# Kernel optimization log

Measured on AMD Instinct MI355X. Metric: run time of the kernel, lower is better.

Reference implementation:

```python
import jax, jax.numpy as jnp
import numpy as np
import math

HIDDEN = 256
INPUT_SIZE = 32

def setup_inputs() -> dict:
    key = jax.random.key(0)
    k1, k2, k3 = jax.random.split(key, 3)
    stdv = 1.0 / math.sqrt(HIDDEN)
    inp = jax.random.normal(k1, (32, 48, 24, INPUT_SIZE), dtype=jnp.float32)
    W = jax.random.uniform(k2, (6 * HIDDEN, INPUT_SIZE + 2 * HIDDEN), minval=-stdv, maxval=stdv, dtype=jnp.float32)
    Bp = jax.random.uniform(k3, (6 * HIDDEN,), minval=-stdv, maxval=stdv, dtype=jnp.float32)
    return {"input": inp, "W": W, "Bp": Bp}

def _witran_forward(input, W, Bp):
    B, rows, cols, C = input.shape
    H = W.shape[0] // 6
    # flag == 1: permute to (cols, batch, rows, C)
    x = jnp.transpose(input, (2, 0, 1, 3))
    R = cols            # Water2sea_slice_num
    Lorig = rows        # Original_slice_len
    L = R + Lorig - 1   # Water2sea_slice_len
    # input_transfer: row r occupies slice positions r : r+Lorig (pad then roll)
    padded = jnp.pad(x, ((0, 0), (0, 0), (0, R - 1), (0, 0)))        # (R, B, L, C)
    shifted = jax.vmap(lambda xr, r: jnp.roll(xr, r, axis=1))(padded, jnp.arange(R))
    a = shifted.reshape(R * B, L, C)
    a_slices = jnp.transpose(a, (1, 0, 2))                            # (L, R*B, C)
    r_idx = jnp.repeat(jnp.arange(R), B)                              # (R*B,)

    def step(carry, inp):
        h_row, h_col = carry
        s, xs = inp
        # bias applied only to first (s+1)*B rows and only while s < R (faithful to torch)
        mask = ((r_idx <= s) & (s < R)).astype(xs.dtype)[:, None]
        gate = jnp.concatenate([h_row, h_col, xs], axis=-1) @ W.T + mask * Bp
        sig = jax.nn.sigmoid(gate[:, : 4 * H])
        tg = jnp.tanh(gate[:, 4 * H:])
        u_row, o_row, u_col, o_col = jnp.split(sig, 4, axis=-1)
        i_row, i_col = jnp.split(tg, 2, axis=-1)
        h_row = jnp.tanh((1.0 - u_row) * h_row + u_row * i_row) * o_row
        h_col_new = jnp.tanh((1.0 - u_col) * h_col + u_col * i_col) * o_col
        # roll col hidden down by one batch block for next diagonal
        h_col_rolled = jnp.roll(h_col_new, B, axis=0)
        return (h_row, h_col_rolled), (h_row, h_col_new)

    init = (jnp.zeros((R * B, H), input.dtype), jnp.zeros((R * B, H), input.dtype))
    _, (rows_all, cols_all) = jax.lax.scan(step, init, (jnp.arange(L), a_slices))
    # output_all_slice: stack along slice dim -> (R*B, L, 2H)
    output_all = jnp.transpose(jnp.concatenate([rows_all, cols_all], axis=-1), (1, 0, 2))
    rows_r = rows_all.reshape(L, R, B, H)
    cols_r = cols_all.reshape(L, R, B, H)
    # row hidden saved at slice s = Lorig-1+k from block k (diagonal)
    hidden_row = rows_r[jnp.arange(Lorig - 1, L), jnp.arange(R)]      # (R, B, H)
    # col hidden saved at slices s >= R-1 from the last block (pre-roll)
    hidden_col = cols_r[R - 1:, R - 1]                                # (Lorig, B, H)
    hidden_row_all = jnp.transpose(hidden_row, (1, 0, 2)).reshape(B, 1, R, H)
    hidden_col_all = jnp.transpose(hidden_col, (1, 0, 2)).reshape(B, 1, Lorig, H)
    # flag == 1 return order: (output, hidden_col_all, hidden_row_all)
    return output_all, hidden_col_all, hidden_row_all

def reference(input, W, Bp):
    return _witran_forward(input, W, Bp)
```

## Files before the change

kernel.cpp:

```cpp
#include <hip/hip_runtime.h>
#include <cstddef>


namespace {
constexpr int H_   = 256;
constexpr int C_   = 32;
constexpr int B_   = 32;
constexpr int R_   = 24;
constexpr int LOR_ = 48;
constexpr int L_   = 71;
constexpr int N_   = 768;
constexpr int KH_  = 512;
constexpr int KT_  = 544;
constexpr int AST_ = 552;
}

typedef __attribute__((ext_vector_type(8))) _Float16       f16x8;
typedef __attribute__((ext_vector_type(8))) unsigned short u16x8;
typedef __attribute__((ext_vector_type(4))) float          f32x4;
typedef __attribute__((ext_vector_type(2))) float          f32x2;

__device__ __forceinline__ float fsig(float x)  { return 1.f / (1.f + __expf(-x)); }
__device__ __forceinline__ float ftanhf(float x){ float e = __expf(2.f * x); return 1.f - 2.f / (e + 1.f); }

__global__ __launch_bounds__(256) void prep_w(const float* __restrict__ W,
                                              _Float16* __restrict__ Wfrag) {
    int o = blockIdx.x * 256 + threadIdx.x;
    int j8   = o & 7;
    int lane = (o >> 3) & 63;
    int rest = o >> 9;
    int lt   = rest % 96;
    int kc   = rest / 96;
    int n0 = lane & 15, quad = lane >> 4;
    int lg  = lt * 16 + n0;
    int kt  = lg / 96;
    int rem = lg % 96;
    int g  = rem >> 4, kl = rem & 15;
    int j  = g * 256 + kt * 16 + kl;
    int kg = kc * 32 + quad * 8 + j8;
    Wfrag[o] = (_Float16)W[j * KT_ + kg];
}

__global__ __launch_bounds__(256) void prep_x(const float* __restrict__ inp,
                                              _Float16* __restrict__ xall) {
    int o = blockIdx.x * 256 + threadIdx.x;
    int c = o & 31;
    int n = (o >> 5) % N_;
    int s = (o >> 5) / N_;
    int r = n >> 5, b = n & 31;
    int l = s - r;
    float v = 0.f;
    if (l >= 0 && l < LOR_) v = inp[((b * LOR_ + l) * R_ + r) * C_ + c];
    xall[o] = (_Float16)v;
}

__global__ __launch_bounds__(384, 2) void step_k(
    const _Float16* __restrict__ Wfrag,
    const _Float16* __restrict__ xall,
    const _Float16* __restrict__ hbc,
    const float*    __restrict__ hfc,
    _Float16*       __restrict__ hbn,
    float*          __restrict__ hfn,
    const float* __restrict__ Bp,
    float* __restrict__ out0, float* __restrict__ out1, float* __restrict__ out2,
    int s)
{
    __shared__ unsigned short As[48 * AST_];
    __shared__ float Gt[48][104];

    const int t    = threadIdx.x;
    const int wv   = t >> 6;
    const int lane = t & 63;
    const int n0   = lane & 15;
    const int quad = lane >> 4;
    const int kt   = blockIdx.x & 15;
    const int mc   = blockIdx.x >> 4;

#pragma unroll
    for (int it = 0; it < 8; ++it) {
        int q   = it * 384 + t;
        int row = q >> 6;
        int col = (q & 63) * 8;
        *(u16x8*)(void*)(&As[row * AST_ + col]) =
            *(const u16x8*)(const void*)((const unsigned short*)hbc +
                                         (size_t)(mc * 48 + row) * KH_ + col);
    }
    if (t < 192) {
        int row = t >> 2;
        int col = (t & 3) * 8;
        *(u16x8*)(void*)(&As[row * AST_ + 512 + col]) =
            *(const u16x8*)(const void*)((const unsigned short*)xall +
                                         (size_t)(s * N_ + mc * 48 + row) * C_ + col);
    }
    __syncthreads();

    f32x4 acc[3];
#pragma unroll
    for (int mt = 0; mt < 3; ++mt) acc[mt] = (f32x4){0.f, 0.f, 0.f, 0.f};

#pragma unroll
    for (int kc = 0; kc < 17; ++kc) {
        f16x8 b = *(const f16x8*)(const void*)(
            Wfrag + ((size_t)(kc * 96 + kt * 6 + wv) * 64 + lane) * 8);
        f16x8 a[3];
#pragma unroll
        for (int mt = 0; mt < 3; ++mt)
            a[mt] = *(const f16x8*)(const void*)(
                &As[(mt * 16 + n0) * AST_ + kc * 32 + quad * 8]);
#pragma unroll
        for (int mt = 0; mt < 3; ++mt)
            acc[mt] = __builtin_amdgcn_mfma_f32_16x16x32_f16(a[mt], b, acc[mt], 0, 0, 0);
    }

#pragma unroll
    for (int mt = 0; mt < 3; ++mt)
#pragma unroll
        for (int reg = 0; reg < 4; ++reg)
            Gt[mt * 16 + quad * 4 + reg][wv * 16 + n0] = acc[mt][reg];

    __syncthreads();

    {
        const int mm = t >> 3;
        const int kp = (t & 7) * 2;
        const int n  = mc * 48 + mm;
        const int k  = kt * 16 + kp;
        const int r  = n >> 5, b = n & 31;
        const bool useb = (r <= s) && (s < R_);

        f32x2 gv[6];
#pragma unroll
        for (int g = 0; g < 6; ++g) {
            f32x2 v  = *(const f32x2*)(const void*)&Gt[mm][g * 16 + kp];
            f32x2 bp = *(const f32x2*)(const void*)(Bp + g * 256 + k);
            gv[g] = useb ? (v + bp) : v;
        }

        f32x2 hro = *(const f32x2*)(const void*)(hfc + (size_t)n * KH_ + k);
        f32x2 hco = *(const f32x2*)(const void*)(hfc + (size_t)n * KH_ + 256 + k);

        f32x2 hrv, hcv;
#pragma unroll
        for (int j = 0; j < 2; ++j) {
            float ur = fsig(gv[0][j]);
            float oR = fsig(gv[1][j]);
            float uc = fsig(gv[2][j]);
            float oc = fsig(gv[3][j]);
            float ir = ftanhf(gv[4][j]);
            float ic = ftanhf(gv[5][j]);
            hrv[j] = ftanhf((1.f - ur) * hro[j] + ur * ir) * oR;
            hcv[j] = ftanhf((1.f - uc) * hco[j] + uc * ic) * oc;
        }

        float* o0 = out0 + ((size_t)n * L_ + s) * 512;
        __builtin_nontemporal_store(hrv, (f32x2*)(void*)(o0 + k));
        __builtin_nontemporal_store(hcv, (f32x2*)(void*)(o0 + 256 + k));

        int n2 = n + B_; if (n2 >= N_) n2 -= N_;
        *(f32x2*)(void*)(hfn + (size_t)n  * KH_ + k)       = hrv;
        *(f32x2*)(void*)(hfn + (size_t)n2 * KH_ + 256 + k) = hcv;

        _Float16 hr0 = (_Float16)hrv[0], hr1 = (_Float16)hrv[1];
        _Float16 hc0 = (_Float16)hcv[0], hc1 = (_Float16)hcv[1];
        _Float16* pr = hbn + (size_t)n  * KH_ + k;
        _Float16* pc = hbn + (size_t)n2 * KH_ + 256 + k;
        pr[0] = hr0; pr[1] = hr1;
        pc[0] = hc0; pc[1] = hc1;

        if (s >= LOR_ - 1 && r == s - (LOR_ - 1))
            __builtin_nontemporal_store(hrv, (f32x2*)(void*)(out2 + (size_t)(b * R_ + r) * H_ + k));
        if (r == R_ - 1 && s >= R_ - 1)
            __builtin_nontemporal_store(hcv, (f32x2*)(void*)(out1 + (size_t)(b * LOR_ + (s - (R_ - 1))) * H_ + k));
    }
}

extern "C" void kernel_launch(void* const* d_in, const int* in_sizes, int n_in,
                              void* d_out, int out_size, void* d_ws, size_t ws_size,
                              hipStream_t stream) {
    const float* inp = (const float*)d_in[0];
    const float* W   = (const float*)d_in[1];
    const float* Bp  = (const float*)d_in[2];

    float* out0 = (float*)d_out;
    float* out1 = out0 + (size_t)N_ * L_ * 512;
    float* out2 = out1 + (size_t)B_ * LOR_ * H_;

    char* ws = (char*)d_ws;
    _Float16* Wfrag = (_Float16*)(ws);
    _Float16* xall  = (_Float16*)(ws + 1671168);
    _Float16* hbf0  = (_Float16*)(ws + 5160960);
    _Float16* hbf1  = (_Float16*)(ws + 5947392);
    float*    hf0   = (float*)(ws + 6733824);
    float*    hf1   = (float*)(ws + 8306688);

    (void)hipMemsetAsync(hbf0, 0, 786432, stream);
    (void)hipMemsetAsync(hf0,  0, 1572864, stream);

    prep_w<<<3264, 256, 0, stream>>>(W, Wfrag);
    prep_x<<<6816, 256, 0, stream>>>(inp, xall);

    for (int s = 0; s < L_; ++s) {
        const _Float16* hbc = (s & 1) ? hbf1 : hbf0;
        _Float16*       hbn = (s & 1) ? hbf0 : hbf1;
        const float*    hfc = (s & 1) ? hf1 : hf0;
        float*          hfn = (s & 1) ? hf0 : hf1;
        step_k<<<256, 384, 0, stream>>>(Wfrag, xall, hbc, hfc, hbn, hfn,
                                        Bp, out0, out1, out2, s);
    }
}
```

Before: 672.7 us.

## Fuse recurrent steps into one persistent kernel with neighbor-only counter sync

Replaces 71 per-step kernel launches with a single persistent kernel that loops over all steps. Blocks synchronize through per-step atomic counters, waiting only on the three row-chunk neighbors whose hidden state they read. Hidden state is exchanged through agent-scope relaxed atomic loads and stores. This is meant to remove launch overhead and full-grid barriers, at the cost of spin-waiting and of depending on all 256 blocks being co-resident. Correctness relies on relaxed atomics plus the barrier giving the needed ordering.

```diff
diff --git a/kernel.cpp b/kernel.cpp
--- a/kernel.cpp
+++ b/kernel.cpp
@@ -22,6 +22,15 @@
 
 __device__ __forceinline__ float fsig(float x)  { return 1.f / (1.f + __expf(-x)); }
 __device__ __forceinline__ float ftanhf(float x){ float e = __expf(2.f * x); return 1.f - 2.f / (e + 1.f); }
+
+__device__ __forceinline__ unsigned long long ld_agent64(const void* p) {
+    return __hip_atomic_load((const unsigned long long*)p,
+                             __ATOMIC_RELAXED, __HIP_MEMORY_SCOPE_AGENT);
+}
+__device__ __forceinline__ void st_agent64(void* p, unsigned long long v) {
+    __hip_atomic_store((unsigned long long*)p, v,
+                       __ATOMIC_RELAXED, __HIP_MEMORY_SCOPE_AGENT);
+}
 
 __global__ __launch_bounds__(256) void prep_w(const float* __restrict__ W,
                                               _Float16* __restrict__ Wfrag) {
@@ -54,16 +63,14 @@
     xall[o] = (_Float16)v;
 }
 
-__global__ __launch_bounds__(384, 2) void step_k(
+__global__ __launch_bounds__(384, 2) void steps_all(
     const _Float16* __restrict__ Wfrag,
     const _Float16* __restrict__ xall,
-    const _Float16* __restrict__ hbc,
-    const float*    __restrict__ hfc,
-    _Float16*       __restrict__ hbn,
-    float*          __restrict__ hfn,
+    _Float16* __restrict__ hb0, _Float16* __restrict__ hb1,
+    float*    __restrict__ hf0, float*    __restrict__ hf1,
     const float* __restrict__ Bp,
     float* __restrict__ out0, float* __restrict__ out1, float* __restrict__ out2,
-    int s)
+    unsigned int* __restrict__ cnt)
 {
     __shared__ unsigned short As[48 * AST_];
     __shared__ float Gt[48][104];
@@ -75,102 +82,133 @@
     const int quad = lane >> 4;
     const int kt   = blockIdx.x & 15;
     const int mc   = blockIdx.x >> 4;
-
-#pragma unroll
-    for (int it = 0; it < 8; ++it) {
-        int q   = it * 384 + t;
-        int row = q >> 6;
-        int col = (q & 63) * 8;
-        *(u16x8*)(void*)(&As[row * AST_ + col]) =
-            *(const u16x8*)(const void*)((const unsigned short*)hbc +
-                                         (size_t)(mc * 48 + row) * KH_ + col);
-    }
-    if (t < 192) {
-        int row = t >> 2;
-        int col = (t & 3) * 8;
-        *(u16x8*)(void*)(&As[row * AST_ + 512 + col]) =
-            *(const u16x8*)(const void*)((const unsigned short*)xall +
-                                         (size_t)(s * N_ + mc * 48 + row) * C_ + col);
-    }
-    __syncthreads();
-
-    f32x4 acc[3];
-#pragma unroll
-    for (int mt = 0; mt < 3; ++mt) acc[mt] = (f32x4){0.f, 0.f, 0.f, 0.f};
-
-#pragma unroll
-    for (int kc = 0; kc < 17; ++kc) {
-        f16x8 b = *(const f16x8*)(const void*)(
-            Wfrag + ((size_t)(kc * 96 + kt * 6 + wv) * 64 + lane) * 8);
-        f16x8 a[3];
+    const int mcm  = (mc + 15) & 15;
+    const int mcp  = (mc + 1) & 15;
+
+    for (int s = 0; s < L_; ++s) {
+        if (s > 0) {
+            if (t == 0) {
+                const unsigned base = (unsigned)(s - 1) * 16u;
+                int guard = 0;
+                for (;;) {
+                    unsigned a = __hip_atomic_load(cnt + base + mcm, __ATOMIC_RELAXED, __HIP_MEMORY_SCOPE_AGENT);
+                    unsigned b = __hip_atomic_load(cnt + base + mc , __ATOMIC_RELAXED, __HIP_MEMORY_SCOPE_AGENT);
+                    unsigned c = __hip_atomic_load(cnt + base + mcp, __ATOMIC_RELAXED, __HIP_MEMORY_SCOPE_AGENT);
+                    if (a >= 16u && b >= 16u && c >= 16u) break;
+                    __builtin_amdgcn_s_sleep(1);
+                    if (++guard > (1 << 24)) break;
+                }
+            }
+            __syncthreads();
+        }
+
+        const _Float16* hbc = (s & 1) ? hb1 : hb0;
+        _Float16*       hbn = (s & 1) ? hb0 : hb1;
+        const float*    hfc = (s & 1) ? hf1 : hf0;
+        float*          hfn = (s & 1) ? hf0 : hf1;
+
+#pragma unroll
+        for (int it = 0; it < 16; ++it) {
+            int q   = it * 384 + t;
+            int row = q >> 7;
+            int c4  = (q & 127) * 4;
+            unsigned long long v = ld_agent64(
+                (const unsigned short*)hbc + (size_t)(mc * 48 + row) * KH_ + c4);
+            *(unsigned long long*)(void*)(&As[row * AST_ + c4]) = v;
+        }
+        if (t < 192) {
+            int row = t >> 2;
+            int col = (t & 3) * 8;
+            *(u16x8*)(void*)(&As[row * AST_ + 512 + col]) =
+                *(const u16x8*)(const void*)((const unsigned short*)xall +
+                                             (size_t)(s * N_ + mc * 48 + row) * C_ + col);
+        }
+        __syncthreads();
+
+        f32x4 acc[3];
+#pragma unroll
+        for (int mt = 0; mt < 3; ++mt) acc[mt] = (f32x4){0.f, 0.f, 0.f, 0.f};
+
+#pragma unroll
+        for (int kc = 0; kc < 17; ++kc) {
+            f16x8 b = *(const f16x8*)(const void*)(
+                Wfrag + ((size_t)(kc * 96 + kt * 6 + wv) * 64 + lane) * 8);
+            f16x8 a[3];
+#pragma unroll
+            for (int mt = 0; mt < 3; ++mt)
+                a[mt] = *(const f16x8*)(const void*)(
+                    &As[(mt * 16 + n0) * AST_ + kc * 32 + quad * 8]);
+#pragma unroll
+            for (int mt = 0; mt < 3; ++mt)
+                acc[mt] = __builtin_amdgcn_mfma_f32_16x16x32_f16(a[mt], b, acc[mt], 0, 0, 0);
+        }
+
 #pragma unroll
         for (int mt = 0; mt < 3; ++mt)
-            a[mt] = *(const f16x8*)(const void*)(
-                &As[(mt * 16 + n0) * AST_ + kc * 32 + quad * 8]);
-#pragma unroll
-        for (int mt = 0; mt < 3; ++mt)
-            acc[mt] = __builtin_amdgcn_mfma_f32_16x16x32_f16(a[mt], b, acc[mt], 0, 0, 0);
-    }
-
-#pragma unroll
-    for (int mt = 0; mt < 3; ++mt)
-#pragma unroll
-        for (int reg = 0; reg < 4; ++reg)
-            Gt[mt * 16 + quad * 4 + reg][wv * 16 + n0] = acc[mt][reg];
-
-    __syncthreads();
-
-    {
-        const int mm = t >> 3;
-        const int kp = (t & 7) * 2;
-        const int n  = mc * 48 + mm;
-        const int k  = kt * 16 + kp;
-        const int r  = n >> 5, b = n & 31;
-        const bool useb = (r <= s) && (s < R_);
-
-        f32x2 gv[6];
-#pragma unroll
-        for (int g = 0; g < 6; ++g) {
-            f32x2 v  = *(const f32x2*)(const void*)&Gt[mm][g * 16 + kp];
-            f32x2 bp = *(const f32x2*)(const void*)(Bp + g * 256 + k);
-            gv[g] = useb ? (v + bp) : v;
-        }
-
-        f32x2 hro = *(const f32x2*)(const void*)(hfc + (size_t)n * KH_ + k);
-        f32x2 hco = *(const f32x2*)(const void*)(hfc + (size_t)n * KH_ + 256 + k);
-
-        f32x2 hrv, hcv;
-#pragma unroll
-        for (int j = 0; j < 2; ++j) {
-            float ur = fsig(gv[0][j]);
-            float oR = fsig(gv[1][j]);
-            float uc = fsig(gv[2][j]);
-            float oc = fsig(gv[3][j]);
-            float ir = ftanhf(gv[4][j]);
-            float ic = ftanhf(gv[5][j]);
-            hrv[j] = ftanhf((1.f - ur) * hro[j] + ur * ir) * oR;
-            hcv[j] = ftanhf((1.f - uc) * hco[j] + uc * ic) * oc;
-        }
-
-        float* o0 = out0 + ((size_t)n * L_ + s) * 512;
-        __builtin_nontemporal_store(hrv, (f32x2*)(void*)(o0 + k));
-        __builtin_nontemporal_store(hcv, (f32x2*)(void*)(o0 + 256 + k));
-
-        int n2 = n + B_; if (n2 >= N_) n2 -= N_;
-        *(f32x2*)(void*)(hfn + (size_t)n  * KH_ + k)       = hrv;
-        *(f32x2*)(void*)(hfn + (size_t)n2 * KH_ + 256 + k) = hcv;
-
-        _Float16 hr0 = (_Float16)hrv[0], hr1 = (_Float16)hrv[1];
-        _Float16 hc0 = (_Float16)hcv[0], hc1 = (_Float16)hcv[1];
-        _Float16* pr = hbn + (size_t)n  * KH_ + k;
-        _Float16* pc = hbn + (size_t)n2 * KH_ + 256 + k;
-        pr[0] = hr0; pr[1] = hr1;
-        pc[0] = hc0; pc[1] = hc1;
-
-        if (s >= LOR_ - 1 && r == s - (LOR_ - 1))
-            __builtin_nontemporal_store(hrv, (f32x2*)(void*)(out2 + (size_t)(b * R_ + r) * H_ + k));
-        if (r == R_ - 1 && s >= R_ - 1)
-            __builtin_nontemporal_store(hcv, (f32x2*)(void*)(out1 + (size_t)(b * LOR_ + (s - (R_ - 1))) * H_ + k));
+#pragma unroll
+            for (int reg = 0; reg < 4; ++reg)
+                Gt[mt * 16 + quad * 4 + reg][wv * 16 + n0] = acc[mt][reg];
+
+        __syncthreads();
+
+        {
+            const int mm = t >> 3;
+            const int kp = (t & 7) * 2;
+            const int n  = mc * 48 + mm;
+            const int k  = kt * 16 + kp;
+            const int r  = n >> 5, b = n & 31;
+            const bool useb = (r <= s) && (s < R_);
+
+            f32x2 gv[6];
+#pragma unroll
+            for (int g = 0; g < 6; ++g) {
+                f32x2 v  = *(const f32x2*)(const void*)&Gt[mm][g * 16 + kp];
+                f32x2 bp = *(const f32x2*)(const void*)(Bp + g * 256 + k);
+                gv[g] = useb ? (v + bp) : v;
+            }
+
+            f32x2 hro = __builtin_bit_cast(f32x2, ld_agent64(hfc + (size_t)n * KH_ + k));
+            f32x2 hco = __builtin_bit_cast(f32x2, ld_agent64(hfc + (size_t)n * KH_ + 256 + k));
+
+            f32x2 hrv, hcv;
+#pragma unroll
+            for (int j = 0; j < 2; ++j) {
+                float ur = fsig(gv[0][j]);
+                float oR = fsig(gv[1][j]);
+                float uc = fsig(gv[2][j]);
+                float oc = fsig(gv[3][j]);
+                float ir = ftanhf(gv[4][j]);
+                float ic = ftanhf(gv[5][j]);
+                hrv[j] = ftanhf((1.f - ur) * hro[j] + ur * ir) * oR;
+                hcv[j] = ftanhf((1.f - uc) * hco[j] + uc * ic) * oc;
+            }
+
+            float* o0 = out0 + ((size_t)n * L_ + s) * 512;
+            __builtin_nontemporal_store(hrv, (f32x2*)(void*)(o0 + k));
+            __builtin_nontemporal_store(hcv, (f32x2*)(void*)(o0 + 256 + k));
+
+            int n2 = n + B_; if (n2 >= N_) n2 -= N_;
+            st_agent64(hfn + (size_t)n  * KH_ + k,       __builtin_bit_cast(unsigned long long, hrv));
+            st_agent64(hfn + (size_t)n2 * KH_ + 256 + k, __builtin_bit_cast(unsigned long long, hcv));
+
+            union { _Float16 h[2]; unsigned int u; } pr, pc;
+            pr.h[0] = (_Float16)hrv[0]; pr.h[1] = (_Float16)hrv[1];
+            pc.h[0] = (_Float16)hcv[0]; pc.h[1] = (_Float16)hcv[1];
+            __hip_atomic_store((unsigned int*)(hbn + (size_t)n  * KH_ + k),       pr.u,
+                               __ATOMIC_RELAXED, __HIP_MEMORY_SCOPE_AGENT);
+            __hip_atomic_store((unsigned int*)(hbn + (size_t)n2 * KH_ + 256 + k), pc.u,
+                               __ATOMIC_RELAXED, __HIP_MEMORY_SCOPE_AGENT);
+
+            if (s >= LOR_ - 1 && r == s - (LOR_ - 1))
+                __builtin_nontemporal_store(hrv, (f32x2*)(void*)(out2 + (size_t)(b * R_ + r) * H_ + k));
+            if (r == R_ - 1 && s >= R_ - 1)
+                __builtin_nontemporal_store(hcv, (f32x2*)(void*)(out1 + (size_t)(b * LOR_ + (s - (R_ - 1))) * H_ + k));
+        }
+
+        __syncthreads();
+        if (t == 0 && s + 1 < L_)
+            __hip_atomic_fetch_add(cnt + (unsigned)s * 16u + mc, 1u,
+                                   __ATOMIC_RELAXED, __HIP_MEMORY_SCOPE_AGENT);
     }
 }
 
@@ -188,23 +226,19 @@
     char* ws = (char*)d_ws;
     _Float16* Wfrag = (_Float16*)(ws);
     _Float16* xall  = (_Float16*)(ws + 1671168);
-    _Float16* hbf0  = (_Float16*)(ws + 5160960);
-    _Float16* hbf1  = (_Float16*)(ws + 5947392);
+    _Float16* hb0   = (_Float16*)(ws + 5160960);
+    _Float16* hb1   = (_Float16*)(ws + 5947392);
     float*    hf0   = (float*)(ws + 6733824);
     float*    hf1   = (float*)(ws + 8306688);
-
-    (void)hipMemsetAsync(hbf0, 0, 786432, stream);
-    (void)hipMemsetAsync(hf0,  0, 1572864, stream);
+    unsigned int* cnt = (unsigned int*)(ws + 9879552);
+
+    (void)hipMemsetAsync(hb0, 0, 786432, stream);
+    (void)hipMemsetAsync(hf0, 0, 1572864, stream);
+    (void)hipMemsetAsync(cnt, 0, 4544, stream);
 
     prep_w<<<3264, 256, 0, stream>>>(W, Wfrag);
     prep_x<<<6816, 256, 0, stream>>>(inp, xall);
 
-    for (int s = 0; s < L_; ++s) {
-        const _Float16* hbc = (s & 1) ? hbf1 : hbf0;
-        _Float16*       hbn = (s & 1) ? hbf0 : hbf1;
-        const float*    hfc = (s & 1) ? hf1 : hf0;
-        float*          hfn = (s & 1) ? hf0 : hf1;
-        step_k<<<256, 384, 0, stream>>>(Wfrag, xall, hbc, hfc, hbn, hfn,
-                                        Bp, out0, out1, out2, s);
-    }
-}
+    steps_all<<<256, 384, 0, stream>>>(Wfrag, xall, hb0, hb1, hf0, hf1,
+                                       Bp, out0, out1, out2, cnt);
+}
```

New measurement: 1.516 ms. +125.4%, slower.

## Halve row tile to double block count and fuse prep kernels with zeroing

Applied to the files above, without the earlier changes.

Shrinks the per-block row tile from 48 to 24 so each recurrent step launches 512 blocks instead of 256, and raises the occupancy hint. This spreads the latency-bound per-step work across more CUs. The price is MFMA work wasted on padding rows and the weight fragments being re-read twice as often. The W and x prep kernels and the two memsets are merged into one launch, and the bias and previous-hidden loads are issued before the GEMM to hide their latency.

```diff
diff --git a/kernel.cpp b/kernel.cpp
--- a/kernel.cpp
+++ b/kernel.cpp
@@ -13,6 +13,7 @@
 constexpr int KH_  = 512;
 constexpr int KT_  = 544;
 constexpr int AST_ = 552;
+constexpr int BM_  = 24;
 }
 
 typedef __attribute__((ext_vector_type(8))) _Float16       f16x8;
@@ -23,38 +24,47 @@
 __device__ __forceinline__ float fsig(float x)  { return 1.f / (1.f + __expf(-x)); }
 __device__ __forceinline__ float ftanhf(float x){ float e = __expf(2.f * x); return 1.f - 2.f / (e + 1.f); }
 
-__global__ __launch_bounds__(256) void prep_w(const float* __restrict__ W,
-                                              _Float16* __restrict__ Wfrag) {
-    int o = blockIdx.x * 256 + threadIdx.x;
-    int j8   = o & 7;
-    int lane = (o >> 3) & 63;
-    int rest = o >> 9;
-    int lt   = rest % 96;
-    int kc   = rest / 96;
-    int n0 = lane & 15, quad = lane >> 4;
-    int lg  = lt * 16 + n0;
-    int kt  = lg / 96;
-    int rem = lg % 96;
-    int g  = rem >> 4, kl = rem & 15;
-    int j  = g * 256 + kt * 16 + kl;
-    int kg = kc * 32 + quad * 8 + j8;
-    Wfrag[o] = (_Float16)W[j * KT_ + kg];
-}
-
-__global__ __launch_bounds__(256) void prep_x(const float* __restrict__ inp,
-                                              _Float16* __restrict__ xall) {
-    int o = blockIdx.x * 256 + threadIdx.x;
-    int c = o & 31;
-    int n = (o >> 5) % N_;
-    int s = (o >> 5) / N_;
-    int r = n >> 5, b = n & 31;
-    int l = s - r;
-    float v = 0.f;
-    if (l >= 0 && l < LOR_) v = inp[((b * LOR_ + l) * R_ + r) * C_ + c];
-    xall[o] = (_Float16)v;
-}
-
-__global__ __launch_bounds__(384, 2) void step_k(
+__global__ __launch_bounds__(256) void prep_all(const float* __restrict__ W,
+                                                const float* __restrict__ inp,
+                                                _Float16* __restrict__ Wfrag,
+                                                _Float16* __restrict__ xall,
+                                                unsigned long long* __restrict__ zb,
+                                                unsigned long long* __restrict__ zf) {
+    const int bx = blockIdx.x;
+    const int t  = threadIdx.x;
+    if (bx < 3264) {
+        int o = bx * 256 + t;
+        int j8   = o & 7;
+        int lane = (o >> 3) & 63;
+        int rest = o >> 9;
+        int lt   = rest % 96;
+        int kc   = rest / 96;
+        int n0 = lane & 15, quad = lane >> 4;
+        int lg  = lt * 16 + n0;
+        int kt  = lg / 96;
+        int rem = lg % 96;
+        int g  = rem >> 4, kl = rem & 15;
+        int j  = g * 256 + kt * 16 + kl;
+        int kg = kc * 32 + quad * 8 + j8;
+        Wfrag[o] = (_Float16)W[j * KT_ + kg];
+    } else if (bx < 10080) {
+        int o = (bx - 3264) * 256 + t;
+        int c = o & 31;
+        int n = (o >> 5) % N_;
+        int s = (o >> 5) / N_;
+        int r = n >> 5, b = n & 31;
+        int l = s - r;
+        float v = 0.f;
+        if (l >= 0 && l < LOR_) v = inp[((b * LOR_ + l) * R_ + r) * C_ + c];
+        xall[o] = (_Float16)v;
+    } else if (bx < 10464) {
+        zb[(bx - 10080) * 256 + t] = 0ull;
+    } else {
+        zf[(bx - 10464) * 256 + t] = 0ull;
+    }
+}
+
+__global__ __launch_bounds__(384, 3) void step_k(
     const _Float16* __restrict__ Wfrag,
     const _Float16* __restrict__ xall,
     const _Float16* __restrict__ hbc,
@@ -65,8 +75,8 @@
     float* __restrict__ out0, float* __restrict__ out1, float* __restrict__ out2,
     int s)
 {
-    __shared__ unsigned short As[48 * AST_];
-    __shared__ float Gt[48][104];
+    __shared__ unsigned short As[32 * AST_];
+    __shared__ float Gt[24][98];
 
     const int t    = threadIdx.x;
     const int wv   = t >> 6;
@@ -76,68 +86,73 @@
     const int kt   = blockIdx.x & 15;
     const int mc   = blockIdx.x >> 4;
 
-#pragma unroll
-    for (int it = 0; it < 8; ++it) {
+    const int mm = t >> 3;
+    const int kp = (t & 7) * 2;
+    const int n  = mc * BM_ + mm;
+    const int k  = kt * 16 + kp;
+    f32x2 bp[6], hro, hco;
+    if (t < 192) {
+#pragma unroll
+        for (int g = 0; g < 6; ++g)
+            bp[g] = *(const f32x2*)(const void*)(Bp + g * 256 + k);
+        hro = *(const f32x2*)(const void*)(hfc + (size_t)n * KH_ + k);
+        hco = *(const f32x2*)(const void*)(hfc + (size_t)n * KH_ + 256 + k);
+    }
+
+#pragma unroll
+    for (int it = 0; it < 4; ++it) {
         int q   = it * 384 + t;
         int row = q >> 6;
         int col = (q & 63) * 8;
         *(u16x8*)(void*)(&As[row * AST_ + col]) =
             *(const u16x8*)(const void*)((const unsigned short*)hbc +
-                                         (size_t)(mc * 48 + row) * KH_ + col);
-    }
-    if (t < 192) {
+                                         (size_t)(mc * BM_ + row) * KH_ + col);
+    }
+    if (t < 96) {
         int row = t >> 2;
         int col = (t & 3) * 8;
         *(u16x8*)(void*)(&As[row * AST_ + 512 + col]) =
             *(const u16x8*)(const void*)((const unsigned short*)xall +
-                                         (size_t)(s * N_ + mc * 48 + row) * C_ + col);
+                                         (size_t)(s * N_ + mc * BM_ + row) * C_ + col);
     }
     __syncthreads();
 
-    f32x4 acc[3];
-#pragma unroll
-    for (int mt = 0; mt < 3; ++mt) acc[mt] = (f32x4){0.f, 0.f, 0.f, 0.f};
+    f32x4 acc0 = (f32x4){0.f, 0.f, 0.f, 0.f};
+    f32x4 acc1 = (f32x4){0.f, 0.f, 0.f, 0.f};
 
 #pragma unroll
     for (int kc = 0; kc < 17; ++kc) {
         f16x8 b = *(const f16x8*)(const void*)(
             Wfrag + ((size_t)(kc * 96 + kt * 6 + wv) * 64 + lane) * 8);
-        f16x8 a[3];
-#pragma unroll
-        for (int mt = 0; mt < 3; ++mt)
-            a[mt] = *(const f16x8*)(const void*)(
-                &As[(mt * 16 + n0) * AST_ + kc * 32 + quad * 8]);
-#pragma unroll
-        for (int mt = 0; mt < 3; ++mt)
-            acc[mt] = __builtin_amdgcn_mfma_f32_16x16x32_f16(a[mt], b, acc[mt], 0, 0, 0);
-    }
-
-#pragma unroll
-    for (int mt = 0; mt < 3; ++mt)
+        f16x8 a0 = *(const f16x8*)(const void*)(
+            &As[(n0) * AST_ + kc * 32 + quad * 8]);
+        f16x8 a1 = *(const f16x8*)(const void*)(
+            &As[(16 + n0) * AST_ + kc * 32 + quad * 8]);
+        acc0 = __builtin_amdgcn_mfma_f32_16x16x32_f16(a0, b, acc0, 0, 0, 0);
+        acc1 = __builtin_amdgcn_mfma_f32_16x16x32_f16(a1, b, acc1, 0, 0, 0);
+    }
+
+#pragma unroll
+    for (int reg = 0; reg < 4; ++reg)
+        Gt[quad * 4 + reg][wv * 16 + n0] = acc0[reg];
+    if (quad < 2) {
 #pragma unroll
         for (int reg = 0; reg < 4; ++reg)
-            Gt[mt * 16 + quad * 4 + reg][wv * 16 + n0] = acc[mt][reg];
+            Gt[16 + quad * 4 + reg][wv * 16 + n0] = acc1[reg];
+    }
 
     __syncthreads();
 
-    {
-        const int mm = t >> 3;
-        const int kp = (t & 7) * 2;
-        const int n  = mc * 48 + mm;
-        const int k  = kt * 16 + kp;
+    if (t < 192) {
         const int r  = n >> 5, b = n & 31;
         const bool useb = (r <= s) && (s < R_);
 
         f32x2 gv[6];
 #pragma unroll
         for (int g = 0; g < 6; ++g) {
-            f32x2 v  = *(const f32x2*)(const void*)&Gt[mm][g * 16 + kp];
-            f32x2 bp = *(const f32x2*)(const void*)(Bp + g * 256 + k);
-            gv[g] = useb ? (v + bp) : v;
+            f32x2 v = *(const f32x2*)(const void*)&Gt[mm][g * 16 + kp];
+            gv[g] = useb ? (v + bp[g]) : v;
         }
-
-        f32x2 hro = *(const f32x2*)(const void*)(hfc + (size_t)n * KH_ + k);
-        f32x2 hco = *(const f32x2*)(const void*)(hfc + (size_t)n * KH_ + 256 + k);
 
         f32x2 hrv, hcv;
 #pragma unroll
@@ -160,12 +175,10 @@
         *(f32x2*)(void*)(hfn + (size_t)n  * KH_ + k)       = hrv;
         *(f32x2*)(void*)(hfn + (size_t)n2 * KH_ + 256 + k) = hcv;
 
-        _Float16 hr0 = (_Float16)hrv[0], hr1 = (_Float16)hrv[1];
-        _Float16 hc0 = (_Float16)hcv[0], hc1 = (_Float16)hcv[1];
         _Float16* pr = hbn + (size_t)n  * KH_ + k;
         _Float16* pc = hbn + (size_t)n2 * KH_ + 256 + k;
-        pr[0] = hr0; pr[1] = hr1;
-        pc[0] = hc0; pc[1] = hc1;
+        pr[0] = (_Float16)hrv[0]; pr[1] = (_Float16)hrv[1];
+        pc[0] = (_Float16)hcv[0]; pc[1] = (_Float16)hcv[1];
 
         if (s >= LOR_ - 1 && r == s - (LOR_ - 1))
             __builtin_nontemporal_store(hrv, (f32x2*)(void*)(out2 + (size_t)(b * R_ + r) * H_ + k));
@@ -188,23 +201,21 @@
     char* ws = (char*)d_ws;
     _Float16* Wfrag = (_Float16*)(ws);
     _Float16* xall  = (_Float16*)(ws + 1671168);
-    _Float16* hbf0  = (_Float16*)(ws + 5160960);
-    _Float16* hbf1  = (_Float16*)(ws + 5947392);
+    _Float16* hb0   = (_Float16*)(ws + 5160960);
+    _Float16* hb1   = (_Float16*)(ws + 5947392);
     float*    hf0   = (float*)(ws + 6733824);
     float*    hf1   = (float*)(ws + 8306688);
 
-    (void)hipMemsetAsync(hbf0, 0, 786432, stream);
-    (void)hipMemsetAsync(hf0,  0, 1572864, stream);
-
-    prep_w<<<3264, 256, 0, stream>>>(W, Wfrag);
-    prep_x<<<6816, 256, 0, stream>>>(inp, xall);
+    prep_all<<<11232, 256, 0, stream>>>(W, inp, Wfrag, xall,
+                                        (unsigned long long*)hb0,
+                                        (unsigned long long*)hf0);
 
     for (int s = 0; s < L_; ++s) {
-        const _Float16* hbc = (s & 1) ? hbf1 : hbf0;
-        _Float16*       hbn = (s & 1) ? hbf0 : hbf1;
+        const _Float16* hbc = (s & 1) ? hb1 : hb0;
+        _Float16*       hbn = (s & 1) ? hb0 : hb1;
         const float*    hfc = (s & 1) ? hf1 : hf0;
         float*          hfn = (s & 1) ? hf0 : hf1;
-        step_k<<<256, 384, 0, stream>>>(Wfrag, xall, hbc, hfc, hbn, hfn,
+        step_k<<<512, 384, 0, stream>>>(Wfrag, xall, hbc, hfc, hbn, hfn,
                                         Bp, out0, out1, out2, s);
     }
 }
```

Result: slower. 687.8 us (+2.2%).

## Drop fp32 hidden state, reuse fp16 LDS copy, preload W fragments, fuse prep kernels

Applied to the files above, without the earlier changes.

Removes the fp32 hidden-state double buffer and instead reads the previous hidden values from the fp16 copy already staged in shared memory, cutting global reads and writes per step. W fragments and bias are loaded into registers before the LDS staging so their latency overlaps. The two prep kernels and the memsets are merged into one launch that also zeroes the initial buffer. The recurrence now carries its hidden state in fp16 only, which adds rounding error to the state.

```diff
diff --git a/kernel.cpp b/kernel.cpp
--- a/kernel.cpp
+++ b/kernel.cpp
@@ -23,50 +23,54 @@
 __device__ __forceinline__ float fsig(float x)  { return 1.f / (1.f + __expf(-x)); }
 __device__ __forceinline__ float ftanhf(float x){ float e = __expf(2.f * x); return 1.f - 2.f / (e + 1.f); }
 
-__global__ __launch_bounds__(256) void prep_w(const float* __restrict__ W,
-                                              _Float16* __restrict__ Wfrag) {
-    int o = blockIdx.x * 256 + threadIdx.x;
-    int j8   = o & 7;
-    int lane = (o >> 3) & 63;
-    int rest = o >> 9;
-    int lt   = rest % 96;
-    int kc   = rest / 96;
-    int n0 = lane & 15, quad = lane >> 4;
-    int lg  = lt * 16 + n0;
-    int kt  = lg / 96;
-    int rem = lg % 96;
-    int g  = rem >> 4, kl = rem & 15;
-    int j  = g * 256 + kt * 16 + kl;
-    int kg = kc * 32 + quad * 8 + j8;
-    Wfrag[o] = (_Float16)W[j * KT_ + kg];
-}
-
-__global__ __launch_bounds__(256) void prep_x(const float* __restrict__ inp,
-                                              _Float16* __restrict__ xall) {
-    int o = blockIdx.x * 256 + threadIdx.x;
-    int c = o & 31;
-    int n = (o >> 5) % N_;
-    int s = (o >> 5) / N_;
-    int r = n >> 5, b = n & 31;
-    int l = s - r;
-    float v = 0.f;
-    if (l >= 0 && l < LOR_) v = inp[((b * LOR_ + l) * R_ + r) * C_ + c];
-    xall[o] = (_Float16)v;
+__global__ __launch_bounds__(256) void prep_all(const float* __restrict__ W,
+                                                const float* __restrict__ inp,
+                                                _Float16* __restrict__ Wfrag,
+                                                _Float16* __restrict__ xall,
+                                                unsigned long long* __restrict__ zb) {
+    const int bx = blockIdx.x;
+    const int t  = threadIdx.x;
+    if (bx < 3264) {
+        int o = bx * 256 + t;
+        int j8   = o & 7;
+        int lane = (o >> 3) & 63;
+        int rest = o >> 9;
+        int lt   = rest % 96;
+        int kc   = rest / 96;
+        int n0 = lane & 15, quad = lane >> 4;
+        int lg  = lt * 16 + n0;
+        int kt  = lg / 96;
+        int rem = lg % 96;
+        int g  = rem >> 4, kl = rem & 15;
+        int j  = g * 256 + kt * 16 + kl;
+        int kg = kc * 32 + quad * 8 + j8;
+        Wfrag[o] = (_Float16)W[j * KT_ + kg];
+    } else if (bx < 10080) {
+        int o = (bx - 3264) * 256 + t;
+        int c = o & 31;
+        int n = (o >> 5) % N_;
+        int s = (o >> 5) / N_;
+        int r = n >> 5, b = n & 31;
+        int l = s - r;
+        float v = 0.f;
+        if (l >= 0 && l < LOR_) v = inp[((b * LOR_ + l) * R_ + r) * C_ + c];
+        xall[o] = (_Float16)v;
+    } else {
+        zb[(bx - 10080) * 256 + t] = 0ull;
+    }
 }
 
 __global__ __launch_bounds__(384, 2) void step_k(
     const _Float16* __restrict__ Wfrag,
     const _Float16* __restrict__ xall,
     const _Float16* __restrict__ hbc,
-    const float*    __restrict__ hfc,
     _Float16*       __restrict__ hbn,
-    float*          __restrict__ hfn,
     const float* __restrict__ Bp,
     float* __restrict__ out0, float* __restrict__ out1, float* __restrict__ out2,
     int s)
 {
     __shared__ unsigned short As[48 * AST_];
-    __shared__ float Gt[48][104];
+    __shared__ float Gt[48][98];
 
     const int t    = threadIdx.x;
     const int wv   = t >> 6;
@@ -76,6 +80,23 @@
     const int kt   = blockIdx.x & 15;
     const int mc   = blockIdx.x >> 4;
 
+    f16x8 bfr[17];
+#pragma unroll
+    for (int kc = 0; kc < 17; ++kc)
+        bfr[kc] = *(const f16x8*)(const void*)(
+            Wfrag + ((size_t)(kc * 96 + kt * 6 + wv) * 64 + lane) * 8);
+
+    const int mm = t >> 3;
+    const int kp = (t & 7) * 2;
+    const int n  = mc * 48 + mm;
+    const int k  = kt * 16 + kp;
+    f32x2 bp[6];
+    if (s < R_) {
+#pragma unroll
+        for (int g = 0; g < 6; ++g)
+            bp[g] = *(const f32x2*)(const void*)(Bp + g * 256 + k);
+    }
+
 #pragma unroll
     for (int it = 0; it < 8; ++it) {
         int q   = it * 384 + t;
@@ -100,8 +121,6 @@
 
 #pragma unroll
     for (int kc = 0; kc < 17; ++kc) {
-        f16x8 b = *(const f16x8*)(const void*)(
-            Wfrag + ((size_t)(kc * 96 + kt * 6 + wv) * 64 + lane) * 8);
         f16x8 a[3];
 #pragma unroll
         for (int mt = 0; mt < 3; ++mt)
@@ -109,7 +128,7 @@
                 &As[(mt * 16 + n0) * AST_ + kc * 32 + quad * 8]);
 #pragma unroll
         for (int mt = 0; mt < 3; ++mt)
-            acc[mt] = __builtin_amdgcn_mfma_f32_16x16x32_f16(a[mt], b, acc[mt], 0, 0, 0);
+            acc[mt] = __builtin_amdgcn_mfma_f32_16x16x32_f16(a[mt], bfr[kc], acc[mt], 0, 0, 0);
     }
 
 #pragma unroll
@@ -121,23 +140,20 @@
     __syncthreads();
 
     {
-        const int mm = t >> 3;
-        const int kp = (t & 7) * 2;
-        const int n  = mc * 48 + mm;
-        const int k  = kt * 16 + kp;
         const int r  = n >> 5, b = n & 31;
         const bool useb = (r <= s) && (s < R_);
 
         f32x2 gv[6];
 #pragma unroll
         for (int g = 0; g < 6; ++g) {
-            f32x2 v  = *(const f32x2*)(const void*)&Gt[mm][g * 16 + kp];
-            f32x2 bp = *(const f32x2*)(const void*)(Bp + g * 256 + k);
-            gv[g] = useb ? (v + bp) : v;
+            f32x2 v = *(const f32x2*)(const void*)&Gt[mm][g * 16 + kp];
+            gv[g] = useb ? (v + bp[g]) : v;
         }
 
-        f32x2 hro = *(const f32x2*)(const void*)(hfc + (size_t)n * KH_ + k);
-        f32x2 hco = *(const f32x2*)(const void*)(hfc + (size_t)n * KH_ + 256 + k);
+        const _Float16* hrow = (const _Float16*)(const void*)&As[mm * AST_ + k];
+        const _Float16* hcol = (const _Float16*)(const void*)&As[mm * AST_ + 256 + k];
+        f32x2 hro = { (float)hrow[0], (float)hrow[1] };
+        f32x2 hco = { (float)hcol[0], (float)hcol[1] };
 
         f32x2 hrv, hcv;
 #pragma unroll
@@ -157,15 +173,12 @@
         __builtin_nontemporal_store(hcv, (f32x2*)(void*)(o0 + 256 + k));
 
         int n2 = n + B_; if (n2 >= N_) n2 -= N_;
-        *(f32x2*)(void*)(hfn + (size_t)n  * KH_ + k)       = hrv;
-        *(f32x2*)(void*)(hfn + (size_t)n2 * KH_ + 256 + k) = hcv;
-
-        _Float16 hr0 = (_Float16)hrv[0], hr1 = (_Float16)hrv[1];
-        _Float16 hc0 = (_Float16)hcv[0], hc1 = (_Float16)hcv[1];
-        _Float16* pr = hbn + (size_t)n  * KH_ + k;
-        _Float16* pc = hbn + (size_t)n2 * KH_ + 256 + k;
-        pr[0] = hr0; pr[1] = hr1;
-        pc[0] = hc0; pc[1] = hc1;
+
+        union { _Float16 h[2]; unsigned int u; } pr, pc;
+        pr.h[0] = (_Float16)hrv[0]; pr.h[1] = (_Float16)hrv[1];
+        pc.h[0] = (_Float16)hcv[0]; pc.h[1] = (_Float16)hcv[1];
+        *(unsigned int*)(void*)(hbn + (size_t)n  * KH_ + k)       = pr.u;
+        *(unsigned int*)(void*)(hbn + (size_t)n2 * KH_ + 256 + k) = pc.u;
 
         if (s >= LOR_ - 1 && r == s - (LOR_ - 1))
             __builtin_nontemporal_store(hrv, (f32x2*)(void*)(out2 + (size_t)(b * R_ + r) * H_ + k));
@@ -188,23 +201,16 @@
     char* ws = (char*)d_ws;
     _Float16* Wfrag = (_Float16*)(ws);
     _Float16* xall  = (_Float16*)(ws + 1671168);
-    _Float16* hbf0  = (_Float16*)(ws + 5160960);
-    _Float16* hbf1  = (_Float16*)(ws + 5947392);
-    float*    hf0   = (float*)(ws + 6733824);
-    float*    hf1   = (float*)(ws + 8306688);
-
-    (void)hipMemsetAsync(hbf0, 0, 786432, stream);
-    (void)hipMemsetAsync(hf0,  0, 1572864, stream);
-
-    prep_w<<<3264, 256, 0, stream>>>(W, Wfrag);
-    prep_x<<<6816, 256, 0, stream>>>(inp, xall);
+    _Float16* hb0   = (_Float16*)(ws + 5160960);
+    _Float16* hb1   = (_Float16*)(ws + 5947392);
+
+    prep_all<<<10464, 256, 0, stream>>>(W, inp, Wfrag, xall,
+                                        (unsigned long long*)hb0);
 
     for (int s = 0; s < L_; ++s) {
-        const _Float16* hbc = (s & 1) ? hbf1 : hbf0;
-        _Float16*       hbn = (s & 1) ? hbf0 : hbf1;
-        const float*    hfc = (s & 1) ? hf1 : hf0;
-        float*          hfn = (s & 1) ? hf0 : hf1;
-        step_k<<<256, 384, 0, stream>>>(Wfrag, xall, hbc, hfc, hbn, hfn,
+        const _Float16* hbc = (s & 1) ? hb1 : hb0;
+        _Float16*       hbn = (s & 1) ? hb0 : hb1;
+        step_k<<<256, 384, 0, stream>>>(Wfrag, xall, hbc, hbn,
                                         Bp, out0, out1, out2, s);
     }
 }
```

After: 629.4 us. 6.4% less time.
